# Kernel tuning notes

Measured on AMD Instinct MI355X. Metric: run time of the kernel, lower is better.

The kernel has to match this reference:

```python
import jax, jax.numpy as jnp
import numpy as np

B, N, DH = 256, 32, 128      # batch, n_agents, per-agent hidden
E = 496                       # n_edges (fully connected over 32 agents)
DIM_IN = 2 * DH               # 256, MLP input (concat of two agent states)
DIM_HID = 256
A = 12                        # dim_act
R = 4                         # payoff_rank
DIM_OUT = 2 * R * A           # 96


def setup_inputs() -> dict:
    key = jax.random.key(0)
    ks = jax.random.split(key, 7)
    hidden_states_n = jax.random.normal(ks[0], (B, N, DH), dtype=jnp.float32)
    edges_from = jax.random.randint(ks[1], (E,), 0, N, dtype=jnp.int32).astype(jnp.int64)
    edges_to = jax.random.randint(ks[2], (E,), 0, N, dtype=jnp.int32).astype(jnp.int64)
    # torch.nn.Linear params: W [out, in], b [out]
    W1 = jax.random.normal(ks[3], (DIM_HID, DIM_IN), dtype=jnp.float32) * (1.0 / np.sqrt(DIM_IN))
    b1 = jnp.zeros((DIM_HID,), dtype=jnp.float32)
    W2 = jax.random.normal(ks[4], (DIM_OUT, DIM_HID), dtype=jnp.float32) * (1.0 / np.sqrt(DIM_HID))
    b2 = jnp.zeros((DIM_OUT,), dtype=jnp.float32)
    return {"hidden_states_n": hidden_states_n, "W1": W1, "b1": b1, "W2": W2,
            "b2": b2, "edges_from": edges_from, "edges_to": edges_to}


def reference(hidden_states_n, W1, b1, W2, b2, edges_from, edges_to):
    hf = hidden_states_n[:, edges_from]                     # [B, E, DH]
    ht = hidden_states_n[:, edges_to]                       # [B, E, DH]
    # stack of (from||to, to||from): [2, B, E, 2*DH]
    inp = jnp.stack([jnp.concatenate([hf, ht], axis=-1),
                     jnp.concatenate([ht, hf], axis=-1)], axis=0)
    h = jax.nn.relu(inp @ W1.T + b1)                        # [2, B, E, DIM_HID]
    p = h @ W2.T + b2                                       # [2, B, E, 2*R*A]
    p = p.reshape(2, B, E, R, 2, A)
    # low-rank outer product per rank, summed over ranks: [2, B, E, A, A]
    payoffs = jnp.einsum('sberi,sberj->sbeij', p[..., 0, :], p[..., 1, :])
    # second copy is transposed, then mean over the two directions
    return 0.5 * (payoffs[0] + jnp.swapaxes(payoffs[1], -1, -2))  # [B, E, A, A]
```

## Files before the change

kernel.cpp:

```cpp
#include <hip/hip_runtime.h>

typedef unsigned int uint;
typedef _Float16 f16;

typedef __attribute__((ext_vector_type(8))) _Float16 f16x8;
typedef __attribute__((ext_vector_type(2))) _Float16 f16x2;
typedef __attribute__((ext_vector_type(4))) float f32x4;

#define E_CNT 496

#define W2_STRIDE 264
#define W2_F16 (96 * W2_STRIDE)
#define W2_STAGE_BYTES 52224
#define W2_CHUNKS 51
#define LDS_BYTES 52224

#define PP_STRIDE 136
#define V_OFF 1088
#define PW_F16 2176

__device__ __forceinline__ uint pack2_f16(float lo, float hi) {
    union { f16x2 h; uint u; } r;
    r.h[0] = (_Float16)lo;
    r.h[1] = (_Float16)hi;
    return r.u;
}

__device__ __forceinline__ void load_lds16(const void* g, void* l) {
    __builtin_amdgcn_global_load_lds(
        (const __attribute__((address_space(1))) void*)g,
        (__attribute__((address_space(3))) void*)l, 16, 0, 0);
}

__global__ __launch_bounds__(256) void x_kernel(
    const float* __restrict__ hidden, const float* __restrict__ W1,
    const float* __restrict__ b1, f16* __restrict__ Xout,
    const float* __restrict__ W2, f16* __restrict__ w2h) {
    __shared__ __align__(16) float hs[64 * 132];

    const int tid = threadIdx.x;

    if (blockIdx.x == 512) {
        #pragma unroll
        for (int j = 0; j < 24; ++j) {
            int idx4 = tid + j * 256;
            int n = idx4 >> 6;
            int k = (idx4 & 63) << 2;
            float4 v = *(const float4*)&W2[n * 256 + k];
            uint2 o;
            o.x = pack2_f16(v.x, v.y);
            o.y = pack2_f16(v.z, v.w);
            *(uint2*)&w2h[n * W2_STRIDE + k] = o;
        }
        return;
    }

    const int rowblock = blockIdx.x >> 2;
    const int g = blockIdx.x & 3;
    const int ln = tid & 63;
    const int waveId = tid >> 6;
    const int quad = ln >> 4;
    const int l16 = ln & 15;
    const int row0 = rowblock * 64;

    union FU { uint u[4]; f16x8 v; };
    FU wf[2][4];
    float bh[2][4];
    #pragma unroll
    for (int nt = 0; nt < 2; ++nt) {
        const int t = (g * 4 + waveId) * 2 + nt;
        const int half = t >> 4;
        const int htile = t & 15;
        const float* wrow = W1 + (htile * 16 + l16) * 256 + half * 128 + quad * 8;
        #pragma unroll
        for (int kk = 0; kk < 4; ++kk) {
            float4 v0 = *(const float4*)(wrow + kk * 32);
            float4 v1 = *(const float4*)(wrow + kk * 32 + 4);
            wf[nt][kk].u[0] = pack2_f16(v0.x, v0.y);
            wf[nt][kk].u[1] = pack2_f16(v0.z, v0.w);
            wf[nt][kk].u[2] = pack2_f16(v1.x, v1.y);
            wf[nt][kk].u[3] = pack2_f16(v1.z, v1.w);
        }
        #pragma unroll
        for (int r = 0; r < 4; ++r)
            bh[nt][r] = 0.5f * b1[htile * 16 + quad * 4 + r];
    }

    {
        const float* src = hidden + row0 * 128;
        #pragma unroll
        for (int it = 0; it < 8; ++it) {
            int idx = it * 256 + tid;
            int r = idx >> 5;
            int c4 = idx & 31;
            float4 v = *(const float4*)(src + idx * 4);
            *(float4*)&hs[r * 132 + c4 * 4] = v;
        }
    }
    __syncthreads();

    #pragma unroll
    for (int ch = 0; ch < 4; ++ch) {
        FU hf[4];
        const float* hrow = &hs[(ch * 16 + l16) * 132 + quad * 8];
        #pragma unroll
        for (int kk = 0; kk < 4; ++kk) {
            float4 v0 = *(const float4*)(hrow + kk * 32);
            float4 v1 = *(const float4*)(hrow + kk * 32 + 4);
            hf[kk].u[0] = pack2_f16(v0.x, v0.y);
            hf[kk].u[1] = pack2_f16(v0.z, v0.w);
            hf[kk].u[2] = pack2_f16(v1.x, v1.y);
            hf[kk].u[3] = pack2_f16(v1.z, v1.w);
        }
        #pragma unroll
        for (int nt = 0; nt < 2; ++nt) {
            const int t = (g * 4 + waveId) * 2 + nt;
            const int half = t >> 4;
            const int htile = t & 15;
            f32x4 acc = (f32x4){0.f, 0.f, 0.f, 0.f};
            #pragma unroll
            for (int kk = 0; kk < 4; ++kk)
                acc = __builtin_amdgcn_mfma_f32_16x16x32_f16(wf[nt][kk].v, hf[kk].v, acc, 0, 0, 0);
            uint2 o;
            o.x = pack2_f16(acc[0] + bh[nt][0], acc[1] + bh[nt][1]);
            o.y = pack2_f16(acc[2] + bh[nt][2], acc[3] + bh[nt][3]);
            f16* dst = Xout + half * (8192 * 256)
                     + (row0 + ch * 16 + l16) * 256 + htile * 16 + quad * 4;
            *(uint2*)dst = o;
        }
    }
}

__global__ __launch_bounds__(512) void gemm_payoff_kernel(
    const f16* __restrict__ X1, const f16* __restrict__ X2,
    const int* __restrict__ e_f, const int* __restrict__ e_t,
    const f16* __restrict__ w2g, const float* __restrict__ b2,
    float* __restrict__ out) {

    __shared__ __align__(16) unsigned char smem[LDS_BYTES];
    f16* w2s = (f16*)smem;

    const int tid = threadIdx.x;
    const int ln = tid & 63;
    const int waveId = tid >> 6;
    const int quad = ln >> 4;
    const int l16 = ln & 15;
    const int pl = l16 & 7;
    const int s = l16 >> 3;

    const int bx = blockIdx.x;
    const int lb = (bx & 7) * 248 + (bx >> 3);

    {
        const unsigned char* src = (const unsigned char*)w2g + ln * 16;
        #pragma unroll
        for (int j = 0; j < 7; ++j) {
            int i = waveId + j * 8;
            if (i < W2_CHUNKS)
                load_lds16(src + i * 1024, smem + i * 1024);
        }
    }

    bool f64 = true, t64 = true;
    #pragma unroll
    for (int i = 0; i < 16; ++i) {
        if (e_f[2 * i + 1] != 0) f64 = false;
        if (e_t[2 * i + 1] != 0) t64 = false;
    }

    const int pairBase = lb * 64 + waveId * 8;
    const f16* px1;
    const f16* px2;
    {
        int pair = pairBase + pl;
        int b = pair / E_CNT;
        int e = pair - b * E_CNT;
        int f = f64 ? e_f[2 * e] : e_f[e];
        int t = t64 ? e_t[2 * e] : e_t[e];
        int n1 = s ? t : f;
        int n2 = s ? f : t;
        px1 = X1 + ((b * 32 + n1) * 256 + quad * 8);
        px2 = X2 + ((b * 32 + n2) * 256 + quad * 8);
    }

    float b2v[6];
    #pragma unroll
    for (int tt = 0; tt < 6; ++tt) b2v[tt] = b2[tt * 16 + l16];

    int d6[6];
    float psc[6];
    {
        const int s_ = quad >> 1;
        #pragma unroll
        for (int tt = 0; tt < 6; ++tt) {
            int n = tt * 16 + l16;
            int rr = n / 24;
            int rem = n - rr * 24;
            int c01 = (rem >= 12) ? 1 : 0;
            int a = rem - c01 * 12;
            int k8 = s_ * 4 + rr;
            int toL = (c01 == s_) ? 1 : 0;
            d6[tt] = (toL ? 0 : V_OFF) + (quad & 1) * 4 * PP_STRIDE + a * 8 + k8;
            psc[tt] = toL ? 0.5f : 1.0f;
        }
    }

    f32x4 acc[6];
    #pragma unroll
    for (int tt = 0; tt < 6; ++tt) acc[tt] = (f32x4){0.f, 0.f, 0.f, 0.f};

    typedef union { uint4 q; f16x8 h; } XU;
    XU G1[2], G2[2];
    G1[0].q = *(const uint4*)(px1 + 0 * 32);
    G2[0].q = *(const uint4*)(px2 + 0 * 32);
    G1[1].q = *(const uint4*)(px1 + 1 * 32);
    G2[1].q = *(const uint4*)(px2 + 1 * 32);

    const f16x8 zero8 = (f16x8){0, 0, 0, 0, 0, 0, 0, 0};

    __syncthreads();

    #pragma unroll
    for (int kk = 0; kk < 8; ++kk) {
        const int buf = kk & 1;
        f16x8 sum = G1[buf].h + G2[buf].h;
        f16x8 af = __builtin_elementwise_max(sum, zero8);
        if (kk < 6) {
            G1[buf].q = *(const uint4*)(px1 + (kk + 2) * 32);
            G2[buf].q = *(const uint4*)(px2 + (kk + 2) * 32);
        }
        #pragma unroll
        for (int tt = 0; tt < 6; ++tt) {
            f16x8 bf = *(const f16x8*)&w2s[(tt * 16 + l16) * W2_STRIDE + kk * 32 + quad * 8];
            acc[tt] = __builtin_amdgcn_mfma_f32_16x16x32_f16(af, bf, acc[tt], 0, 0, 0);
        }
    }

    __syncthreads();

    f16* pm = (f16*)smem + waveId * PW_F16;

    #pragma unroll
    for (int tt = 0; tt < 6; ++tt) {
        #pragma unroll
        for (int r = 0; r < 4; ++r)
            pm[d6[tt] + r * PP_STRIDE] = (_Float16)((acc[tt][r] + b2v[tt]) * psc[tt]);
    }

    #pragma unroll
    for (int pp = 0; pp < 8; ++pp) {
        f16x8 afp = zero8, bfp = zero8;
        if (quad == 0) {
            afp = *(const f16x8*)&pm[V_OFF + pp * PP_STRIDE + l16 * 8];
            bfp = *(const f16x8*)&pm[pp * PP_STRIDE + l16 * 8];
        }
        f32x4 d = __builtin_amdgcn_mfma_f32_16x16x32_f16(
            afp, bfp, (f32x4){0.f, 0.f, 0.f, 0.f}, 0, 0, 0);
        if (l16 < 12 && quad < 3) {
            float* ob = out + (pairBase + pp) * 144 + l16 * 12 + quad * 4;
            *(float4*)ob = make_float4(d[0], d[1], d[2], d[3]);
        }
    }
}

extern "C" void kernel_launch(void* const* d_in, const int* in_sizes, int n_in,
                              void* d_out, int out_size, void* d_ws, size_t ws_size,
                              hipStream_t stream) {
    const float* hidden = (const float*)d_in[0];
    const float* W1 = (const float*)d_in[1];
    const float* b1 = (const float*)d_in[2];
    const float* W2 = (const float*)d_in[3];
    const float* b2 = (const float*)d_in[4];
    const int* e_f = (const int*)d_in[5];
    const int* e_t = (const int*)d_in[6];
    float* out = (float*)d_out;

    char* ws = (char*)d_ws;
    f16* X = (f16*)ws;
    f16* w2h = (f16*)(ws + 8 * 1024 * 1024);

    x_kernel<<<513, 256, 0, stream>>>(hidden, W1, b1, X, W2, w2h);
    gemm_payoff_kernel<<<1984, 512, 0, stream>>>(X, X + 8192 * 256, e_f, e_t, w2h, b2, out);
}
```

Measured before the change: 131.6 us.

## Process two pair groups per wave and stage X output through LDS

The payoff kernel now handles 16 pairs per wave (two 8-pair groups) and halves the grid. This amortizes the per-block W2 LDS staging and reuses each W2 fragment read from LDS across two MFMAs. The first kernel now writes its f16 results to LDS and then stores full contiguous 16-byte rows to global memory, replacing scattered 8-byte writes. In exchange the payoff kernel holds more registers (two accumulator sets and twice the prefetch buffers), which may lower occupancy, and the half-size grid gives fewer blocks to spread across the GPU.

```diff
diff --git a/kernel.cpp b/kernel.cpp
--- a/kernel.cpp
+++ b/kernel.cpp
@@ -10,7 +10,6 @@
 #define E_CNT 496
 
 #define W2_STRIDE 264
-#define W2_F16 (96 * W2_STRIDE)
 #define W2_STAGE_BYTES 52224
 #define W2_CHUNKS 51
 #define LDS_BYTES 52224
@@ -18,6 +17,9 @@
 #define PP_STRIDE 136
 #define V_OFF 1088
 #define PW_F16 2176
+
+#define XK_LDS_BYTES 33792
+#define XS_STRIDE 136
 
 __device__ __forceinline__ uint pack2_f16(float lo, float hi) {
     union { f16x2 h; uint u; } r;
@@ -36,7 +38,9 @@
     const float* __restrict__ hidden, const float* __restrict__ W1,
     const float* __restrict__ b1, f16* __restrict__ Xout,
     const float* __restrict__ W2, f16* __restrict__ w2h) {
-    __shared__ __align__(16) float hs[64 * 132];
+    __shared__ __align__(16) unsigned char xsmem[XK_LDS_BYTES];
+    float* hs = (float*)xsmem;
+    f16* xs = (f16*)xsmem;
 
     const int tid = threadIdx.x;
 
@@ -62,6 +66,8 @@
     const int quad = ln >> 4;
     const int l16 = ln & 15;
     const int row0 = rowblock * 64;
+    const int half = g >> 1;
+    const int hbase = (g & 1) * 128;
 
     union FU { uint u[4]; f16x8 v; };
     FU wf[2][4];
@@ -69,7 +75,6 @@
     #pragma unroll
     for (int nt = 0; nt < 2; ++nt) {
         const int t = (g * 4 + waveId) * 2 + nt;
-        const int half = t >> 4;
         const int htile = t & 15;
         const float* wrow = W1 + (htile * 16 + l16) * 256 + half * 128 + quad * 8;
         #pragma unroll
@@ -99,6 +104,7 @@
     }
     __syncthreads();
 
+    f32x4 accs[4][2];
     #pragma unroll
     for (int ch = 0; ch < 4; ++ch) {
         FU hf[4];
@@ -114,20 +120,37 @@
         }
         #pragma unroll
         for (int nt = 0; nt < 2; ++nt) {
-            const int t = (g * 4 + waveId) * 2 + nt;
-            const int half = t >> 4;
-            const int htile = t & 15;
             f32x4 acc = (f32x4){0.f, 0.f, 0.f, 0.f};
             #pragma unroll
             for (int kk = 0; kk < 4; ++kk)
                 acc = __builtin_amdgcn_mfma_f32_16x16x32_f16(wf[nt][kk].v, hf[kk].v, acc, 0, 0, 0);
+            accs[ch][nt] = acc;
+        }
+    }
+
+    __syncthreads();
+
+    #pragma unroll
+    for (int ch = 0; ch < 4; ++ch) {
+        #pragma unroll
+        for (int nt = 0; nt < 2; ++nt) {
             uint2 o;
-            o.x = pack2_f16(acc[0] + bh[nt][0], acc[1] + bh[nt][1]);
-            o.y = pack2_f16(acc[2] + bh[nt][2], acc[3] + bh[nt][3]);
-            f16* dst = Xout + half * (8192 * 256)
-                     + (row0 + ch * 16 + l16) * 256 + htile * 16 + quad * 4;
-            *(uint2*)dst = o;
-        }
+            o.x = pack2_f16(accs[ch][nt][0] + bh[nt][0], accs[ch][nt][1] + bh[nt][1]);
+            o.y = pack2_f16(accs[ch][nt][2] + bh[nt][2], accs[ch][nt][3] + bh[nt][3]);
+            *(uint2*)&xs[(ch * 16 + l16) * XS_STRIDE + (2 * waveId + nt) * 16 + quad * 4] = o;
+        }
+    }
+
+    __syncthreads();
+
+    f16* xdst = Xout + half * (8192 * 256) + row0 * 256 + hbase;
+    #pragma unroll
+    for (int it = 0; it < 4; ++it) {
+        int idx = it * 256 + tid;
+        int row = idx >> 4;
+        int h8 = idx & 15;
+        uint4 v = *(const uint4*)&xs[row * XS_STRIDE + h8 * 8];
+        *(uint4*)&xdst[row * 256 + h8 * 8] = v;
     }
 }
 
@@ -149,7 +172,7 @@
     const int s = l16 >> 3;
 
     const int bx = blockIdx.x;
-    const int lb = (bx & 7) * 248 + (bx >> 3);
+    const int lb = (bx & 7) * 124 + (bx >> 3);
 
     {
         const unsigned char* src = (const unsigned char*)w2g + ln * 16;
@@ -168,19 +191,64 @@
         if (e_t[2 * i + 1] != 0) t64 = false;
     }
 
-    const int pairBase = lb * 64 + waveId * 8;
-    const f16* px1;
-    const f16* px2;
-    {
-        int pair = pairBase + pl;
+    const int pairBase = lb * 128 + waveId * 16;
+    const f16* px1[2];
+    const f16* px2[2];
+    #pragma unroll
+    for (int c = 0; c < 2; ++c) {
+        int pair = pairBase + c * 8 + pl;
         int b = pair / E_CNT;
         int e = pair - b * E_CNT;
         int f = f64 ? e_f[2 * e] : e_f[e];
         int t = t64 ? e_t[2 * e] : e_t[e];
         int n1 = s ? t : f;
         int n2 = s ? f : t;
-        px1 = X1 + ((b * 32 + n1) * 256 + quad * 8);
-        px2 = X2 + ((b * 32 + n2) * 256 + quad * 8);
+        px1[c] = X1 + ((b * 32 + n1) * 256 + quad * 8);
+        px2[c] = X2 + ((b * 32 + n2) * 256 + quad * 8);
+    }
+
+    f32x4 acc[2][6];
+    #pragma unroll
+    for (int c = 0; c < 2; ++c)
+        #pragma unroll
+        for (int tt = 0; tt < 6; ++tt) acc[c][tt] = (f32x4){0.f, 0.f, 0.f, 0.f};
+
+    typedef union { uint4 q; f16x8 h; } XU;
+    XU G1[2][2], G2[2][2];
+    #pragma unroll
+    for (int c = 0; c < 2; ++c) {
+        G1[0][c].q = *(const uint4*)(px1[c] + 0 * 32);
+        G2[0][c].q = *(const uint4*)(px2[c] + 0 * 32);
+        G1[1][c].q = *(const uint4*)(px1[c] + 1 * 32);
+        G2[1][c].q = *(const uint4*)(px2[c] + 1 * 32);
+    }
+
+    const f16x8 zero8 = (f16x8){0, 0, 0, 0, 0, 0, 0, 0};
+
+    __syncthreads();
+
+    #pragma unroll
+    for (int kk = 0; kk < 8; ++kk) {
+        const int buf = kk & 1;
+        f16x8 af[2];
+        #pragma unroll
+        for (int c = 0; c < 2; ++c) {
+            f16x8 sum = G1[buf][c].h + G2[buf][c].h;
+            af[c] = __builtin_elementwise_max(sum, zero8);
+        }
+        if (kk < 6) {
+            #pragma unroll
+            for (int c = 0; c < 2; ++c) {
+                G1[buf][c].q = *(const uint4*)(px1[c] + (kk + 2) * 32);
+                G2[buf][c].q = *(const uint4*)(px2[c] + (kk + 2) * 32);
+            }
+        }
+        #pragma unroll
+        for (int tt = 0; tt < 6; ++tt) {
+            f16x8 bf = *(const f16x8*)&w2s[(tt * 16 + l16) * W2_STRIDE + kk * 32 + quad * 8];
+            acc[0][tt] = __builtin_amdgcn_mfma_f32_16x16x32_f16(af[0], bf, acc[0][tt], 0, 0, 0);
+            acc[1][tt] = __builtin_amdgcn_mfma_f32_16x16x32_f16(af[1], bf, acc[1][tt], 0, 0, 0);
+        }
     }
 
     float b2v[6];
@@ -205,60 +273,32 @@
         }
     }
 
-    f32x4 acc[6];
-    #pragma unroll
-    for (int tt = 0; tt < 6; ++tt) acc[tt] = (f32x4){0.f, 0.f, 0.f, 0.f};
-
-    typedef union { uint4 q; f16x8 h; } XU;
-    XU G1[2], G2[2];
-    G1[0].q = *(const uint4*)(px1 + 0 * 32);
-    G2[0].q = *(const uint4*)(px2 + 0 * 32);
-    G1[1].q = *(const uint4*)(px1 + 1 * 32);
-    G2[1].q = *(const uint4*)(px2 + 1 * 32);
-
-    const f16x8 zero8 = (f16x8){0, 0, 0, 0, 0, 0, 0, 0};
-
-    __syncthreads();
-
-    #pragma unroll
-    for (int kk = 0; kk < 8; ++kk) {
-        const int buf = kk & 1;
-        f16x8 sum = G1[buf].h + G2[buf].h;
-        f16x8 af = __builtin_elementwise_max(sum, zero8);
-        if (kk < 6) {
-            G1[buf].q = *(const uint4*)(px1 + (kk + 2) * 32);
-            G2[buf].q = *(const uint4*)(px2 + (kk + 2) * 32);
-        }
+    __syncthreads();
+
+    f16* pm = (f16*)smem + waveId * PW_F16;
+
+    #pragma unroll
+    for (int c = 0; c < 2; ++c) {
         #pragma unroll
         for (int tt = 0; tt < 6; ++tt) {
-            f16x8 bf = *(const f16x8*)&w2s[(tt * 16 + l16) * W2_STRIDE + kk * 32 + quad * 8];
-            acc[tt] = __builtin_amdgcn_mfma_f32_16x16x32_f16(af, bf, acc[tt], 0, 0, 0);
-        }
-    }
-
-    __syncthreads();
-
-    f16* pm = (f16*)smem + waveId * PW_F16;
-
-    #pragma unroll
-    for (int tt = 0; tt < 6; ++tt) {
-        #pragma unroll
-        for (int r = 0; r < 4; ++r)
-            pm[d6[tt] + r * PP_STRIDE] = (_Float16)((acc[tt][r] + b2v[tt]) * psc[tt]);
-    }
-
-    #pragma unroll
-    for (int pp = 0; pp < 8; ++pp) {
-        f16x8 afp = zero8, bfp = zero8;
-        if (quad == 0) {
-            afp = *(const f16x8*)&pm[V_OFF + pp * PP_STRIDE + l16 * 8];
-            bfp = *(const f16x8*)&pm[pp * PP_STRIDE + l16 * 8];
-        }
-        f32x4 d = __builtin_amdgcn_mfma_f32_16x16x32_f16(
-            afp, bfp, (f32x4){0.f, 0.f, 0.f, 0.f}, 0, 0, 0);
-        if (l16 < 12 && quad < 3) {
-            float* ob = out + (pairBase + pp) * 144 + l16 * 12 + quad * 4;
-            *(float4*)ob = make_float4(d[0], d[1], d[2], d[3]);
+            #pragma unroll
+            for (int r = 0; r < 4; ++r)
+                pm[d6[tt] + r * PP_STRIDE] = (_Float16)((acc[c][tt][r] + b2v[tt]) * psc[tt]);
+        }
+
+        #pragma unroll
+        for (int pp = 0; pp < 8; ++pp) {
+            f16x8 afp = zero8, bfp = zero8;
+            if (quad == 0) {
+                afp = *(const f16x8*)&pm[V_OFF + pp * PP_STRIDE + l16 * 8];
+                bfp = *(const f16x8*)&pm[pp * PP_STRIDE + l16 * 8];
+            }
+            f32x4 d = __builtin_amdgcn_mfma_f32_16x16x32_f16(
+                afp, bfp, (f32x4){0.f, 0.f, 0.f, 0.f}, 0, 0, 0);
+            if (l16 < 12 && quad < 3) {
+                float* ob = out + (pairBase + c * 8 + pp) * 144 + l16 * 12 + quad * 4;
+                *(float4*)ob = make_float4(d[0], d[1], d[2], d[3]);
+            }
         }
     }
 }
@@ -280,5 +320,5 @@
     f16* w2h = (f16*)(ws + 8 * 1024 * 1024);
 
     x_kernel<<<513, 256, 0, stream>>>(hidden, W1, b1, X, W2, w2h);
-    gemm_payoff_kernel<<<1984, 512, 0, stream>>>(X, X + 8192 * 256, e_f, e_t, w2h, b2, out);
-}
+    gemm_payoff_kernel<<<992, 512, 0, stream>>>(X, X + 8192 * 256, e_f, e_t, w2h, b2, out);
+}
```

Result: no change. 133.8 us (+1.6%).

## Stage X outputs through LDS for coalesced stores; deepen gather prefetch

Applied to the files above, without the earlier changes.

The projection kernel now keeps its MFMA results in registers, writes them to an LDS tile and then stores 16-byte coalesced rows to global memory, instead of issuing scattered 8-byte stores per lane. Each block's column mapping is remapped so it covers a contiguous 128-column slice of one half. The payoff kernel now prefetches four K-chunks of gathered activations instead of two, moves the GEMM ahead of the epilogue index setup, and adds a minimum-occupancy hint to launch bounds. These changes target store coalescing and load latency, at the cost of extra LDS traffic, added barriers, and higher register pressure.

```diff
diff --git a/kernel.cpp b/kernel.cpp
--- a/kernel.cpp
+++ b/kernel.cpp
@@ -10,7 +10,6 @@
 #define E_CNT 496
 
 #define W2_STRIDE 264
-#define W2_F16 (96 * W2_STRIDE)
 #define W2_STAGE_BYTES 52224
 #define W2_CHUNKS 51
 #define LDS_BYTES 52224
@@ -18,6 +17,9 @@
 #define PP_STRIDE 136
 #define V_OFF 1088
 #define PW_F16 2176
+
+#define XK_LDS_BYTES 33792
+#define XS_STRIDE 136
 
 __device__ __forceinline__ uint pack2_f16(float lo, float hi) {
     union { f16x2 h; uint u; } r;
@@ -36,7 +38,9 @@
     const float* __restrict__ hidden, const float* __restrict__ W1,
     const float* __restrict__ b1, f16* __restrict__ Xout,
     const float* __restrict__ W2, f16* __restrict__ w2h) {
-    __shared__ __align__(16) float hs[64 * 132];
+    __shared__ __align__(16) unsigned char xsmem[XK_LDS_BYTES];
+    float* hs = (float*)xsmem;
+    f16* xs = (f16*)xsmem;
 
     const int tid = threadIdx.x;
 
@@ -62,6 +66,8 @@
     const int quad = ln >> 4;
     const int l16 = ln & 15;
     const int row0 = rowblock * 64;
+    const int half = g >> 1;
+    const int hbase = (g & 1) * 128;
 
     union FU { uint u[4]; f16x8 v; };
     FU wf[2][4];
@@ -69,7 +75,6 @@
     #pragma unroll
     for (int nt = 0; nt < 2; ++nt) {
         const int t = (g * 4 + waveId) * 2 + nt;
-        const int half = t >> 4;
         const int htile = t & 15;
         const float* wrow = W1 + (htile * 16 + l16) * 256 + half * 128 + quad * 8;
         #pragma unroll
@@ -99,6 +104,7 @@
     }
     __syncthreads();
 
+    f32x4 accs[4][2];
     #pragma unroll
     for (int ch = 0; ch < 4; ++ch) {
         FU hf[4];
@@ -114,24 +120,41 @@
         }
         #pragma unroll
         for (int nt = 0; nt < 2; ++nt) {
-            const int t = (g * 4 + waveId) * 2 + nt;
-            const int half = t >> 4;
-            const int htile = t & 15;
             f32x4 acc = (f32x4){0.f, 0.f, 0.f, 0.f};
             #pragma unroll
             for (int kk = 0; kk < 4; ++kk)
                 acc = __builtin_amdgcn_mfma_f32_16x16x32_f16(wf[nt][kk].v, hf[kk].v, acc, 0, 0, 0);
+            accs[ch][nt] = acc;
+        }
+    }
+
+    __syncthreads();
+
+    #pragma unroll
+    for (int ch = 0; ch < 4; ++ch) {
+        #pragma unroll
+        for (int nt = 0; nt < 2; ++nt) {
             uint2 o;
-            o.x = pack2_f16(acc[0] + bh[nt][0], acc[1] + bh[nt][1]);
-            o.y = pack2_f16(acc[2] + bh[nt][2], acc[3] + bh[nt][3]);
-            f16* dst = Xout + half * (8192 * 256)
-                     + (row0 + ch * 16 + l16) * 256 + htile * 16 + quad * 4;
-            *(uint2*)dst = o;
-        }
-    }
-}
-
-__global__ __launch_bounds__(512) void gemm_payoff_kernel(
+            o.x = pack2_f16(accs[ch][nt][0] + bh[nt][0], accs[ch][nt][1] + bh[nt][1]);
+            o.y = pack2_f16(accs[ch][nt][2] + bh[nt][2], accs[ch][nt][3] + bh[nt][3]);
+            *(uint2*)&xs[(ch * 16 + l16) * XS_STRIDE + (2 * waveId + nt) * 16 + quad * 4] = o;
+        }
+    }
+
+    __syncthreads();
+
+    f16* xdst = Xout + half * (8192 * 256) + row0 * 256 + hbase;
+    #pragma unroll
+    for (int it = 0; it < 4; ++it) {
+        int idx = it * 256 + tid;
+        int row = idx >> 4;
+        int h8 = idx & 15;
+        uint4 v = *(const uint4*)&xs[row * XS_STRIDE + h8 * 8];
+        *(uint4*)&xdst[row * 256 + h8 * 8] = v;
+    }
+}
+
+__global__ __launch_bounds__(512, 6) void gemm_payoff_kernel(
     const f16* __restrict__ X1, const f16* __restrict__ X2,
     const int* __restrict__ e_f, const int* __restrict__ e_t,
     const f16* __restrict__ w2g, const float* __restrict__ b2,
@@ -183,6 +206,38 @@
         px2 = X2 + ((b * 32 + n2) * 256 + quad * 8);
     }
 
+    f32x4 acc[6];
+    #pragma unroll
+    for (int tt = 0; tt < 6; ++tt) acc[tt] = (f32x4){0.f, 0.f, 0.f, 0.f};
+
+    typedef union { uint4 q; f16x8 h; } XU;
+    XU G1[4], G2[4];
+    #pragma unroll
+    for (int c = 0; c < 4; ++c) {
+        G1[c].q = *(const uint4*)(px1 + c * 32);
+        G2[c].q = *(const uint4*)(px2 + c * 32);
+    }
+
+    const f16x8 zero8 = (f16x8){0, 0, 0, 0, 0, 0, 0, 0};
+
+    __syncthreads();
+
+    #pragma unroll
+    for (int kk = 0; kk < 8; ++kk) {
+        const int buf = kk & 3;
+        f16x8 sum = G1[buf].h + G2[buf].h;
+        f16x8 af = __builtin_elementwise_max(sum, zero8);
+        if (kk < 4) {
+            G1[buf].q = *(const uint4*)(px1 + (kk + 4) * 32);
+            G2[buf].q = *(const uint4*)(px2 + (kk + 4) * 32);
+        }
+        #pragma unroll
+        for (int tt = 0; tt < 6; ++tt) {
+            f16x8 bf = *(const f16x8*)&w2s[(tt * 16 + l16) * W2_STRIDE + kk * 32 + quad * 8];
+            acc[tt] = __builtin_amdgcn_mfma_f32_16x16x32_f16(af, bf, acc[tt], 0, 0, 0);
+        }
+    }
+
     float b2v[6];
     #pragma unroll
     for (int tt = 0; tt < 6; ++tt) b2v[tt] = b2[tt * 16 + l16];
@@ -202,37 +257,6 @@
             int toL = (c01 == s_) ? 1 : 0;
             d6[tt] = (toL ? 0 : V_OFF) + (quad & 1) * 4 * PP_STRIDE + a * 8 + k8;
             psc[tt] = toL ? 0.5f : 1.0f;
-        }
-    }
-
-    f32x4 acc[6];
-    #pragma unroll
-    for (int tt = 0; tt < 6; ++tt) acc[tt] = (f32x4){0.f, 0.f, 0.f, 0.f};
-
-    typedef union { uint4 q; f16x8 h; } XU;
-    XU G1[2], G2[2];
-    G1[0].q = *(const uint4*)(px1 + 0 * 32);
-    G2[0].q = *(const uint4*)(px2 + 0 * 32);
-    G1[1].q = *(const uint4*)(px1 + 1 * 32);
-    G2[1].q = *(const uint4*)(px2 + 1 * 32);
-
-    const f16x8 zero8 = (f16x8){0, 0, 0, 0, 0, 0, 0, 0};
-
-    __syncthreads();
-
-    #pragma unroll
-    for (int kk = 0; kk < 8; ++kk) {
-        const int buf = kk & 1;
-        f16x8 sum = G1[buf].h + G2[buf].h;
-        f16x8 af = __builtin_elementwise_max(sum, zero8);
-        if (kk < 6) {
-            G1[buf].q = *(const uint4*)(px1 + (kk + 2) * 32);
-            G2[buf].q = *(const uint4*)(px2 + (kk + 2) * 32);
-        }
-        #pragma unroll
-        for (int tt = 0; tt < 6; ++tt) {
-            f16x8 bf = *(const f16x8*)&w2s[(tt * 16 + l16) * W2_STRIDE + kk * 32 + quad * 8];
-            acc[tt] = __builtin_amdgcn_mfma_f32_16x16x32_f16(af, bf, acc[tt], 0, 0, 0);
         }
     }
 
```

After: 132.2 us. No clear change (+0.5%).

## Use 32x32x16 MFMA with 16 pairs per wave and LDS-staged X output

Applied to the files above, without the earlier changes.

The main GEMM kernel moves from 16x16x32 MFMAs over 8 edge-pairs per wave to 32x32x16 MFMAs over 16 edge-pairs per wave. This halves the block count and doubles the work per block, so each W2 tile staged in LDS is reused across more pairs. The payoff scatter layout in LDS is reworked to match the new accumulator layout. The first kernel now has each block compute a full 128-column half of X, staging the result in LDS so it can write coalesced 16-byte rows, with half as many blocks, each taking on more work.

```diff
diff --git a/kernel.cpp b/kernel.cpp
--- a/kernel.cpp
+++ b/kernel.cpp
@@ -6,18 +6,21 @@
 typedef __attribute__((ext_vector_type(8))) _Float16 f16x8;
 typedef __attribute__((ext_vector_type(2))) _Float16 f16x2;
 typedef __attribute__((ext_vector_type(4))) float f32x4;
+typedef __attribute__((ext_vector_type(16))) float f32x16;
 
 #define E_CNT 496
 
 #define W2_STRIDE 264
-#define W2_F16 (96 * W2_STRIDE)
 #define W2_STAGE_BYTES 52224
 #define W2_CHUNKS 51
-#define LDS_BYTES 52224
-
-#define PP_STRIDE 136
-#define V_OFF 1088
-#define PW_F16 2176
+#define LDS_BYTES 53248
+
+#define PP_STRIDE 104
+#define V_OFF 1664
+#define PW_BYTES 6656
+
+#define XS_STRIDE 264
+#define XH_BYTES 33792
 
 __device__ __forceinline__ uint pack2_f16(float lo, float hi) {
     union { f16x2 h; uint u; } r;
@@ -36,11 +39,13 @@
     const float* __restrict__ hidden, const float* __restrict__ W1,
     const float* __restrict__ b1, f16* __restrict__ Xout,
     const float* __restrict__ W2, f16* __restrict__ w2h) {
-    __shared__ __align__(16) float hs[64 * 132];
+    __shared__ __align__(16) unsigned char xsmem[XH_BYTES + 64 * XS_STRIDE * 2];
+    float* hs = (float*)xsmem;
+    f16* xs = (f16*)(xsmem + XH_BYTES);
 
     const int tid = threadIdx.x;
 
-    if (blockIdx.x == 512) {
+    if (blockIdx.x == 256) {
         #pragma unroll
         for (int j = 0; j < 24; ++j) {
             int idx4 = tid + j * 256;
@@ -55,36 +60,13 @@
         return;
     }
 
-    const int rowblock = blockIdx.x >> 2;
-    const int g = blockIdx.x & 3;
+    const int rowblock = blockIdx.x >> 1;
+    const int half = blockIdx.x & 1;
     const int ln = tid & 63;
     const int waveId = tid >> 6;
     const int quad = ln >> 4;
     const int l16 = ln & 15;
     const int row0 = rowblock * 64;
-
-    union FU { uint u[4]; f16x8 v; };
-    FU wf[2][4];
-    float bh[2][4];
-    #pragma unroll
-    for (int nt = 0; nt < 2; ++nt) {
-        const int t = (g * 4 + waveId) * 2 + nt;
-        const int half = t >> 4;
-        const int htile = t & 15;
-        const float* wrow = W1 + (htile * 16 + l16) * 256 + half * 128 + quad * 8;
-        #pragma unroll
-        for (int kk = 0; kk < 4; ++kk) {
-            float4 v0 = *(const float4*)(wrow + kk * 32);
-            float4 v1 = *(const float4*)(wrow + kk * 32 + 4);
-            wf[nt][kk].u[0] = pack2_f16(v0.x, v0.y);
-            wf[nt][kk].u[1] = pack2_f16(v0.z, v0.w);
-            wf[nt][kk].u[2] = pack2_f16(v1.x, v1.y);
-            wf[nt][kk].u[3] = pack2_f16(v1.z, v1.w);
-        }
-        #pragma unroll
-        for (int r = 0; r < 4; ++r)
-            bh[nt][r] = 0.5f * b1[htile * 16 + quad * 4 + r];
-    }
 
     {
         const float* src = hidden + row0 * 128;
@@ -99,35 +81,68 @@
     }
     __syncthreads();
 
-    #pragma unroll
-    for (int ch = 0; ch < 4; ++ch) {
-        FU hf[4];
-        const float* hrow = &hs[(ch * 16 + l16) * 132 + quad * 8];
-        #pragma unroll
-        for (int kk = 0; kk < 4; ++kk) {
-            float4 v0 = *(const float4*)(hrow + kk * 32);
-            float4 v1 = *(const float4*)(hrow + kk * 32 + 4);
-            hf[kk].u[0] = pack2_f16(v0.x, v0.y);
-            hf[kk].u[1] = pack2_f16(v0.z, v0.w);
-            hf[kk].u[2] = pack2_f16(v1.x, v1.y);
-            hf[kk].u[3] = pack2_f16(v1.z, v1.w);
-        }
+    union FU { uint u[4]; f16x8 v; };
+
+    #pragma unroll
+    for (int p = 0; p < 2; ++p) {
+        FU wf[2][4];
+        float bh[2][4];
         #pragma unroll
         for (int nt = 0; nt < 2; ++nt) {
-            const int t = (g * 4 + waveId) * 2 + nt;
-            const int half = t >> 4;
-            const int htile = t & 15;
-            f32x4 acc = (f32x4){0.f, 0.f, 0.f, 0.f};
+            const int tl = p * 8 + waveId * 2 + nt;
+            const float* wrow = W1 + (tl * 16 + l16) * 256 + half * 128 + quad * 8;
             #pragma unroll
-            for (int kk = 0; kk < 4; ++kk)
-                acc = __builtin_amdgcn_mfma_f32_16x16x32_f16(wf[nt][kk].v, hf[kk].v, acc, 0, 0, 0);
-            uint2 o;
-            o.x = pack2_f16(acc[0] + bh[nt][0], acc[1] + bh[nt][1]);
-            o.y = pack2_f16(acc[2] + bh[nt][2], acc[3] + bh[nt][3]);
-            f16* dst = Xout + half * (8192 * 256)
-                     + (row0 + ch * 16 + l16) * 256 + htile * 16 + quad * 4;
-            *(uint2*)dst = o;
-        }
+            for (int kk = 0; kk < 4; ++kk) {
+                float4 v0 = *(const float4*)(wrow + kk * 32);
+                float4 v1 = *(const float4*)(wrow + kk * 32 + 4);
+                wf[nt][kk].u[0] = pack2_f16(v0.x, v0.y);
+                wf[nt][kk].u[1] = pack2_f16(v0.z, v0.w);
+                wf[nt][kk].u[2] = pack2_f16(v1.x, v1.y);
+                wf[nt][kk].u[3] = pack2_f16(v1.z, v1.w);
+            }
+            #pragma unroll
+            for (int r = 0; r < 4; ++r)
+                bh[nt][r] = 0.5f * b1[tl * 16 + quad * 4 + r];
+        }
+
+        #pragma unroll
+        for (int ch = 0; ch < 4; ++ch) {
+            FU hf[4];
+            const float* hrow = &hs[(ch * 16 + l16) * 132 + quad * 8];
+            #pragma unroll
+            for (int kk = 0; kk < 4; ++kk) {
+                float4 v0 = *(const float4*)(hrow + kk * 32);
+                float4 v1 = *(const float4*)(hrow + kk * 32 + 4);
+                hf[kk].u[0] = pack2_f16(v0.x, v0.y);
+                hf[kk].u[1] = pack2_f16(v0.z, v0.w);
+                hf[kk].u[2] = pack2_f16(v1.x, v1.y);
+                hf[kk].u[3] = pack2_f16(v1.z, v1.w);
+            }
+            #pragma unroll
+            for (int nt = 0; nt < 2; ++nt) {
+                const int tl = p * 8 + waveId * 2 + nt;
+                f32x4 acc = (f32x4){0.f, 0.f, 0.f, 0.f};
+                #pragma unroll
+                for (int kk = 0; kk < 4; ++kk)
+                    acc = __builtin_amdgcn_mfma_f32_16x16x32_f16(wf[nt][kk].v, hf[kk].v, acc, 0, 0, 0);
+                uint2 o;
+                o.x = pack2_f16(acc[0] + bh[nt][0], acc[1] + bh[nt][1]);
+                o.y = pack2_f16(acc[2] + bh[nt][2], acc[3] + bh[nt][3]);
+                *(uint2*)&xs[(ch * 16 + l16) * XS_STRIDE + tl * 16 + quad * 4] = o;
+            }
+        }
+    }
+
+    __syncthreads();
+
+    f16* xdst = Xout + half * (8192 * 256) + row0 * 256;
+    #pragma unroll
+    for (int it = 0; it < 8; ++it) {
+        int idx = it * 256 + tid;
+        int row = idx >> 5;
+        int c8 = idx & 31;
+        uint4 v = *(const uint4*)&xs[row * XS_STRIDE + c8 * 8];
+        *(uint4*)&xdst[row * 256 + c8 * 8] = v;
     }
 }
 
@@ -143,13 +158,13 @@
     const int tid = threadIdx.x;
     const int ln = tid & 63;
     const int waveId = tid >> 6;
+    const int l32 = ln & 31;
+    const int khalf = ln >> 5;
     const int quad = ln >> 4;
     const int l16 = ln & 15;
-    const int pl = l16 & 7;
-    const int s = l16 >> 3;
 
     const int bx = blockIdx.x;
-    const int lb = (bx & 7) * 248 + (bx >> 3);
+    const int lb = (bx & 7) * 124 + (bx >> 3);
 
     {
         const unsigned char* src = (const unsigned char*)w2g + ln * 16;
@@ -168,87 +183,93 @@
         if (e_t[2 * i + 1] != 0) t64 = false;
     }
 
-    const int pairBase = lb * 64 + waveId * 8;
+    const int pairBase = lb * 128 + waveId * 16;
     const f16* px1;
     const f16* px2;
     {
-        int pair = pairBase + pl;
+        int p = ln & 15;
+        int sdim = (ln >> 4) & 1;
+        int pair = pairBase + p;
         int b = pair / E_CNT;
         int e = pair - b * E_CNT;
         int f = f64 ? e_f[2 * e] : e_f[e];
         int t = t64 ? e_t[2 * e] : e_t[e];
-        int n1 = s ? t : f;
-        int n2 = s ? f : t;
-        px1 = X1 + ((b * 32 + n1) * 256 + quad * 8);
-        px2 = X2 + ((b * 32 + n2) * 256 + quad * 8);
-    }
-
-    float b2v[6];
-    #pragma unroll
-    for (int tt = 0; tt < 6; ++tt) b2v[tt] = b2[tt * 16 + l16];
-
-    int d6[6];
-    float psc[6];
-    {
-        const int s_ = quad >> 1;
-        #pragma unroll
-        for (int tt = 0; tt < 6; ++tt) {
-            int n = tt * 16 + l16;
-            int rr = n / 24;
-            int rem = n - rr * 24;
-            int c01 = (rem >= 12) ? 1 : 0;
-            int a = rem - c01 * 12;
-            int k8 = s_ * 4 + rr;
-            int toL = (c01 == s_) ? 1 : 0;
-            d6[tt] = (toL ? 0 : V_OFF) + (quad & 1) * 4 * PP_STRIDE + a * 8 + k8;
-            psc[tt] = toL ? 0.5f : 1.0f;
-        }
-    }
-
-    f32x4 acc[6];
-    #pragma unroll
-    for (int tt = 0; tt < 6; ++tt) acc[tt] = (f32x4){0.f, 0.f, 0.f, 0.f};
+        int n1 = sdim ? t : f;
+        int n2 = sdim ? f : t;
+        px1 = X1 + ((b * 32 + n1) * 256 + khalf * 8);
+        px2 = X2 + ((b * 32 + n2) * 256 + khalf * 8);
+    }
+
+    f32x16 acc[3];
+    #pragma unroll
+    for (int tt = 0; tt < 3; ++tt)
+        #pragma unroll
+        for (int j = 0; j < 16; ++j) acc[tt][j] = 0.f;
 
     typedef union { uint4 q; f16x8 h; } XU;
-    XU G1[2], G2[2];
-    G1[0].q = *(const uint4*)(px1 + 0 * 32);
-    G2[0].q = *(const uint4*)(px2 + 0 * 32);
-    G1[1].q = *(const uint4*)(px1 + 1 * 32);
-    G2[1].q = *(const uint4*)(px2 + 1 * 32);
+    XU G1[4], G2[4];
+    #pragma unroll
+    for (int c = 0; c < 4; ++c) {
+        G1[c].q = *(const uint4*)(px1 + c * 16);
+        G2[c].q = *(const uint4*)(px2 + c * 16);
+    }
 
     const f16x8 zero8 = (f16x8){0, 0, 0, 0, 0, 0, 0, 0};
 
     __syncthreads();
 
     #pragma unroll
-    for (int kk = 0; kk < 8; ++kk) {
-        const int buf = kk & 1;
+    for (int kk = 0; kk < 16; ++kk) {
+        const int buf = kk & 3;
         f16x8 sum = G1[buf].h + G2[buf].h;
         f16x8 af = __builtin_elementwise_max(sum, zero8);
-        if (kk < 6) {
-            G1[buf].q = *(const uint4*)(px1 + (kk + 2) * 32);
-            G2[buf].q = *(const uint4*)(px2 + (kk + 2) * 32);
-        }
-        #pragma unroll
-        for (int tt = 0; tt < 6; ++tt) {
-            f16x8 bf = *(const f16x8*)&w2s[(tt * 16 + l16) * W2_STRIDE + kk * 32 + quad * 8];
-            acc[tt] = __builtin_amdgcn_mfma_f32_16x16x32_f16(af, bf, acc[tt], 0, 0, 0);
-        }
+        if (kk < 12) {
+            G1[buf].q = *(const uint4*)(px1 + (kk + 4) * 16);
+            G2[buf].q = *(const uint4*)(px2 + (kk + 4) * 16);
+        }
+        #pragma unroll
+        for (int tt = 0; tt < 3; ++tt) {
+            f16x8 bf = *(const f16x8*)&w2s[(tt * 32 + l32) * W2_STRIDE + kk * 16 + khalf * 8];
+            acc[tt] = __builtin_amdgcn_mfma_f32_32x32x16_f16(af, bf, acc[tt], 0, 0, 0);
+        }
+    }
+
+    float b2n[3];
+    int d0[3], d1[3];
+    float sc0[3], sc1[3];
+    #pragma unroll
+    for (int tt = 0; tt < 3; ++tt) {
+        int n = tt * 32 + l32;
+        b2n[tt] = b2[n];
+        int rr = n / 24;
+        int rem = n - rr * 24;
+        int c01 = (rem >= 12) ? 1 : 0;
+        int a = rem - c01 * 12;
+        int toL0 = (c01 == 0);
+        int toL1 = (c01 == 1);
+        d0[tt] = (toL0 ? 0 : V_OFF) + a * 8 + rr;
+        d1[tt] = (toL1 ? 0 : V_OFF) + a * 8 + 4 + rr;
+        sc0[tt] = toL0 ? 0.5f : 1.0f;
+        sc1[tt] = toL1 ? 0.5f : 1.0f;
     }
 
     __syncthreads();
 
-    f16* pm = (f16*)smem + waveId * PW_F16;
-
-    #pragma unroll
-    for (int tt = 0; tt < 6; ++tt) {
-        #pragma unroll
-        for (int r = 0; r < 4; ++r)
-            pm[d6[tt] + r * PP_STRIDE] = (_Float16)((acc[tt][r] + b2v[tt]) * psc[tt]);
-    }
-
-    #pragma unroll
-    for (int pp = 0; pp < 8; ++pp) {
+    f16* pm = (f16*)(smem + waveId * PW_BYTES);
+
+    #pragma unroll
+    for (int tt = 0; tt < 3; ++tt) {
+        #pragma unroll
+        for (int j = 0; j < 16; ++j) {
+            int pp = (j & 3) + 8 * ((j >> 2) & 1) + 4 * khalf;
+            int dst = ((j >> 3) ? d1[tt] : d0[tt]) + pp * PP_STRIDE;
+            float sc = (j >> 3) ? sc1[tt] : sc0[tt];
+            pm[dst] = (_Float16)((acc[tt][j] + b2n[tt]) * sc);
+        }
+    }
+
+    #pragma unroll
+    for (int pp = 0; pp < 16; ++pp) {
         f16x8 afp = zero8, bfp = zero8;
         if (quad == 0) {
             afp = *(const f16x8*)&pm[V_OFF + pp * PP_STRIDE + l16 * 8];
@@ -279,6 +300,6 @@
     f16* X = (f16*)ws;
     f16* w2h = (f16*)(ws + 8 * 1024 * 1024);
 
-    x_kernel<<<513, 256, 0, stream>>>(hidden, W1, b1, X, W2, w2h);
-    gemm_payoff_kernel<<<1984, 512, 0, stream>>>(X, X + 8192 * 256, e_f, e_t, w2h, b2, out);
-}
+    x_kernel<<<257, 256, 0, stream>>>(hidden, W1, b1, X, W2, w2h);
+    gemm_payoff_kernel<<<992, 512, 0, stream>>>(X, X + 8192 * 256, e_f, e_t, w2h, b2, out);
+}
```

Result: no change. 131.1 us (-0.4%).
